# Performance work log

Hardware: AMD Instinct MI355X
Metric: run time of the kernel (lower is better)

The kernel has to match this reference:

```python
import jax, jax.numpy as jnp
import numpy as np

N_NODES = 4096
N_HEADS = 8
NEG_SLOPE = 0.2  # PyG GATConv default leaky_relu slope


def _gat_single(h, src, dst, att_src, att_dst):
    # h: [N, H, C] projected node features; src/dst: [E] (self-loops included)
    a_s = (h * att_src).sum(-1)                      # [N, H]
    a_d = (h * att_dst).sum(-1)                      # [N, H]
    e = jax.nn.leaky_relu(a_s[src] + a_d[dst], NEG_SLOPE)   # [E, H]
    m = jax.ops.segment_max(e, dst, num_segments=N_NODES)   # [N, H]
    ex = jnp.exp(e - m[dst])                         # [E, H]
    denom = jax.ops.segment_sum(ex, dst, num_segments=N_NODES)
    alpha = ex / denom[dst]                          # [E, H] (self-loops => denom > 0)
    out = jax.ops.segment_sum(alpha[:, :, None] * h[src], dst, num_segments=N_NODES)
    return out                                       # [N, H, C]


def setup_inputs() -> dict:
    key = jax.random.key(0)
    ks = jax.random.split(key, 12)
    B, T, N, F = 4, 12, N_NODES, 8
    Hg, Hl = 64, 128
    inp = {
        "x": jax.random.normal(ks[0], (B, T, N, F), jnp.float32),
        "edge_index": jax.random.randint(ks[1], (2, 65536), 0, N, jnp.int64),
        "W_gat": jax.random.normal(ks[2], (F, Hg), jnp.float32) * 0.3,
        "att_src": jax.random.normal(ks[3], (N_HEADS, Hg // N_HEADS), jnp.float32) * 0.3,
        "att_dst": jax.random.normal(ks[4], (N_HEADS, Hg // N_HEADS), jnp.float32) * 0.3,
        "b_gat": jax.random.normal(ks[5], (Hg,), jnp.float32) * 0.1,
        "W_ih": jax.random.normal(ks[6], (4 * Hl, Hg * N), jnp.float32) * 0.002,
        "W_hh": jax.random.normal(ks[7], (4 * Hl, Hl), jnp.float32) * 0.05,
        "b_ih": jax.random.normal(ks[8], (4 * Hl,), jnp.float32) * 0.05,
        "b_hh": jax.random.normal(ks[9], (4 * Hl,), jnp.float32) * 0.05,
        "W_fc": jax.random.normal(ks[10], (Hl, N * F), jnp.float32) * 0.05,
        "b_fc": jax.random.normal(ks[11], (N * F,), jnp.float32) * 0.05,
    }
    return inp


def reference(x, edge_index, W_gat, att_src, att_dst, b_gat,
              W_ih, W_hh, b_ih, b_hh, W_fc, b_fc):
    B, T, N, F = x.shape
    H = N_HEADS
    C = W_gat.shape[1] // H
    Hl = W_hh.shape[1]

    # add self-loops (PyG GATConv default add_self_loops=True)
    loop = jnp.arange(N, dtype=edge_index.dtype)
    src = jnp.concatenate([edge_index[0], loop])
    dst = jnp.concatenate([edge_index[1], loop])

    # ---- GAT over all (batch, time) graphs at once ----
    h = (x.reshape(B * T, N, F) @ W_gat).reshape(B * T, N, H, C)
    gat = jax.vmap(_gat_single, in_axes=(0, None, None, None, None))(
        h, src, dst, att_src, att_dst)                # [BT, N, H, C]
    gat = gat.reshape(B * T, N, H * C) + b_gat
    gat = jax.nn.elu(gat)                             # dropout p=0 (eval) => identity
    seq = gat.reshape(B, T, N * H * C)

    # ---- LSTM (torch gate order: i, f, g, o) ----
    def step(carry, x_t):
        hprev, cprev = carry
        gates = x_t @ W_ih.T + b_ih + hprev @ W_hh.T + b_hh   # [B, 4Hl]
        i, f, g, o = jnp.split(gates, 4, axis=-1)
        c = jax.nn.sigmoid(f) * cprev + jax.nn.sigmoid(i) * jnp.tanh(g)
        hn = jax.nn.sigmoid(o) * jnp.tanh(c)
        return (hn, c), None

    h0 = jnp.zeros((B, Hl), x.dtype)
    (h_last, _), _ = jax.lax.scan(step, (h0, h0), seq.transpose(1, 0, 2))

    out = h_last @ W_fc + b_fc
    return out.reshape(B, N, F)
```

## Files before the change

kernel.cpp:

```cpp
#include <hip/hip_runtime.h>

#define NN 4096
#define NH 8
#define BTT 48
#define KG 262144
#define NJ 512
#define HLL 128
#define ERAW 65536
#define NKC 256
#define NG  24576
#define CAP 64

typedef __attribute__((ext_vector_type(8))) short bf16x8;
typedef __attribute__((ext_vector_type(4))) float f32x4;
typedef __attribute__((ext_vector_type(8))) unsigned short ushort8;

__device__ __forceinline__ unsigned short f2bf(float f) {
  unsigned int u = __float_as_uint(f);
  u += 0x7FFFu + ((u >> 16) & 1u);
  return (unsigned short)(u >> 16);
}
__device__ __forceinline__ float bf2f(unsigned short s) {
  return __uint_as_float(((unsigned int)s) << 16);
}
__device__ __forceinline__ float4 nt_load4(const float* p) {
  f32x4 v = __builtin_nontemporal_load((const f32x4*)p);
  return float4{v[0], v[1], v[2], v[3]};
}

__global__ __launch_bounds__(256) void k_scatter(const int* __restrict__ ei, int* __restrict__ cursor,
                                                 int* __restrict__ ssrc) {
  int t = blockIdx.x * 256 + threadIdx.x;
  if (t < ERAW) {
    int s = ei[t], d = ei[ERAW + t];
    int pos = atomicAdd(&cursor[d], 1);
    ssrc[(d << 6) + pos] = s;
  } else {
    int n = t - ERAW;
    int pos = atomicAdd(&cursor[n], 1);
    ssrc[(n << 6) + pos] = n;
  }
}

__global__ __launch_bounds__(256) void k_proj(const float* __restrict__ x, const float* __restrict__ Wg,
                                              const float* __restrict__ att_s, const float* __restrict__ att_d,
                                              unsigned short* __restrict__ h, float* __restrict__ a_s,
                                              float* __restrict__ a_d) {
  __shared__ float wgs[512];
  __shared__ float ats[64], atd[64];
  int tid = threadIdx.x;
  wgs[tid] = Wg[tid];
  wgs[256 + tid] = Wg[256 + tid];
  if (tid < 64) { ats[tid] = att_s[tid]; atd[tid] = att_d[tid]; }
  __syncthreads();
  int bt = blockIdx.x >> 7;
  int inner = blockIdx.x & 127;
  int hd = tid & 7, nl = tid >> 3;
  int n = inner * 32 + nl;
  const float* xr = x + ((size_t)(bt * NN + n)) * 8;
  float4 xa = *(const float4*)xr, xb2 = *(const float4*)(xr + 4);
  float xv[8] = {xa.x, xa.y, xa.z, xa.w, xb2.x, xb2.y, xb2.z, xb2.w};
  int hb = hd * 8;
  float hv[8];
#pragma unroll
  for (int c = 0; c < 8; ++c) {
    float acc = 0.f;
#pragma unroll
    for (int f = 0; f < 8; ++f) acc += xv[f] * wgs[f * 64 + hb + c];
    hv[c] = acc;
  }
  float as = 0.f, ad = 0.f;
#pragma unroll
  for (int c = 0; c < 8; ++c) { as += hv[c] * ats[hb + c]; ad += hv[c] * atd[hb + c]; }
  int aoff = bt * (NN * NH) + n * NH + hd;
  a_s[aoff] = as;
  a_d[aoff] = ad;
  ushort8 hr;
#pragma unroll
  for (int c = 0; c < 8; ++c) hr[c] = f2bf(hv[c]);
  *(ushort8*)(h + (size_t)bt * KG + (size_t)n * 64 + hb) = hr;
}

__global__ __launch_bounds__(256) void k_gat(const unsigned short* __restrict__ h, const float* __restrict__ a_s,
                                             const float* __restrict__ a_d, const int* __restrict__ cursor,
                                             const int* __restrict__ ssrc, const float* __restrict__ b_gat,
                                             unsigned short* __restrict__ Xb) {
  int B = blockIdx.x;
  int xcd = B & 7;
  int slot = B >> 3;
  int btg = slot >> 7;
  int inner = slot & 127;
  int bt = btg * 8 + xcd;
  int tid = threadIdx.x;
  int hd = tid & 7, nl = tid >> 3;
  int n = inner * 32 + nl;
  const unsigned short* hbase = h + (size_t)bt * KG;
  const float* asb = a_s + bt * (NN * NH);
  float adn = a_d[bt * (NN * NH) + n * NH + hd];
  int deg = cursor[n];
  const int* bucket = ssrc + (n << 6);
  float ssum = 0.f;
  float o[8];
#pragma unroll
  for (int c = 0; c < 8; ++c) o[c] = 0.f;
  for (int i = 0; i < deg; ++i) {
    int s = bucket[i];
    float e = asb[s * NH + hd] + adn;
    e = (e > 0.f) ? e : 0.2f * e;
    float p = __expf(e);
    ssum += p;
    ushort8 hvv = *(const ushort8*)(hbase + (size_t)s * 64 + hd * 8);
#pragma unroll
    for (int c = 0; c < 8; ++c) o[c] += p * bf2f(hvv[c]);
  }
  float inv = 1.f / ssum;
  ushort8 r;
#pragma unroll
  for (int c = 0; c < 8; ++c) {
    float v = o[c] * inv + b_gat[hd * 8 + c];
    v = (v > 0.f) ? v : (__expf(v) - 1.f);
    r[c] = f2bf(v);
  }
  *(ushort8*)(Xb + (size_t)bt * KG + (size_t)n * 64 + hd * 8) = r;
}

__global__ __launch_bounds__(256) void k_gemm(const unsigned short* __restrict__ Xb,
                                              const float* __restrict__ Wih, float* __restrict__ Gp) {
  int tid = threadIdx.x;
  int w = tid >> 6, lane = tid & 63;
  int lm = lane & 15, kg = lane >> 4;
  int jb = blockIdx.x & 3;
  int kc = blockIdx.x >> 2;
  int j0 = jb * 128 + w * 32;
  size_t kbase = (size_t)kc * 1024 + kg * 8;

  const float* wr0 = Wih + (size_t)(j0 + lm) * KG + kbase;
  const float* wr1 = Wih + (size_t)(j0 + 16 + lm) * KG + kbase;
  const short* Xs = (const short*)Xb;
  const short* xr0 = Xs + (size_t)lm * KG + kbase;
  const short* xr1 = xr0 + (size_t)16 * KG;
  const short* xr2 = xr0 + (size_t)32 * KG;

  f32x4 acc[3][2];
#pragma unroll
  for (int mf = 0; mf < 3; ++mf)
#pragma unroll
    for (int jf = 0; jf < 2; ++jf) acc[mf][jf] = f32x4{0.f, 0.f, 0.f, 0.f};

  float4 wbuf[2][4];
  bf16x8 abuf[2][3];

  wbuf[0][0] = nt_load4(wr0);
  wbuf[0][1] = nt_load4(wr0 + 4);
  wbuf[0][2] = nt_load4(wr1);
  wbuf[0][3] = nt_load4(wr1 + 4);
  abuf[0][0] = *(const bf16x8*)(xr0);
  abuf[0][1] = *(const bf16x8*)(xr1);
  abuf[0][2] = *(const bf16x8*)(xr2);

#pragma unroll 2
  for (int t = 0; t < 32; ++t) {
    int cur = t & 1, nxt = cur ^ 1;
    if (t + 1 < 32) {
      int off = (t + 1) * 32;
      wbuf[nxt][0] = nt_load4(wr0 + off);
      wbuf[nxt][1] = nt_load4(wr0 + off + 4);
      wbuf[nxt][2] = nt_load4(wr1 + off);
      wbuf[nxt][3] = nt_load4(wr1 + off + 4);
      abuf[nxt][0] = *(const bf16x8*)(xr0 + off);
      abuf[nxt][1] = *(const bf16x8*)(xr1 + off);
      abuf[nxt][2] = *(const bf16x8*)(xr2 + off);
    }
#pragma unroll
    for (int jf = 0; jf < 2; ++jf) {
      float4 f0 = wbuf[cur][jf * 2], f1 = wbuf[cur][jf * 2 + 1];
      bf16x8 bb;
      bb[0] = (short)f2bf(f0.x); bb[1] = (short)f2bf(f0.y);
      bb[2] = (short)f2bf(f0.z); bb[3] = (short)f2bf(f0.w);
      bb[4] = (short)f2bf(f1.x); bb[5] = (short)f2bf(f1.y);
      bb[6] = (short)f2bf(f1.z); bb[7] = (short)f2bf(f1.w);
      acc[0][jf] = __builtin_amdgcn_mfma_f32_16x16x32_bf16(abuf[cur][0], bb, acc[0][jf], 0, 0, 0);
      acc[1][jf] = __builtin_amdgcn_mfma_f32_16x16x32_bf16(abuf[cur][1], bb, acc[1][jf], 0, 0, 0);
      acc[2][jf] = __builtin_amdgcn_mfma_f32_16x16x32_bf16(abuf[cur][2], bb, acc[2][jf], 0, 0, 0);
    }
  }

  float* gout = Gp + (size_t)kc * NG;
#pragma unroll
  for (int mf = 0; mf < 3; ++mf)
#pragma unroll
    for (int jf = 0; jf < 2; ++jf) {
      int j = j0 + jf * 16 + lm;
#pragma unroll
      for (int r = 0; r < 4; ++r) {
        int bt = mf * 16 + kg * 4 + r;
        gout[bt * NJ + j] = acc[mf][jf][r];
      }
    }
}

__global__ __launch_bounds__(256) void k_red1(const float* __restrict__ Gp, float* __restrict__ Gp2) {
  int idx = blockIdx.x * 256 + threadIdx.x;
  int seg = idx / NG;
  int gid = idx - seg * NG;
  const float* src = Gp + (size_t)seg * 32 * NG + gid;
  float acc = 0.f;
#pragma unroll 8
  for (int i = 0; i < 32; ++i) acc += src[(size_t)i * NG];
  Gp2[idx] = acc;
}

__global__ __launch_bounds__(512) void k_lstm(const float* __restrict__ Gp2, const float* __restrict__ Whh,
                                              const float* __restrict__ bih, const float* __restrict__ bhh,
                                              float* __restrict__ hlast) {
  __shared__ float hs[HLL];
  __shared__ float gs[NJ];
  int b = blockIdx.x, j = threadIdx.x;
  float bias = bih[j] + bhh[j];
  float w[HLL];
  const float* wr = Whh + (size_t)j * HLL;
#pragma unroll
  for (int k = 0; k < HLL; k += 4) {
    float4 v = *(const float4*)(wr + k);
    w[k] = v.x; w[k + 1] = v.y; w[k + 2] = v.z; w[k + 3] = v.w;
  }
  if (j < HLL) hs[j] = 0.f;
  float c = 0.f;
  __syncthreads();
  for (int t = 0; t < 12; ++t) {
    const float* gp = Gp2 + (size_t)(b * 12 + t) * NJ + j;
    float acc = bias;
#pragma unroll
    for (int s = 0; s < 8; ++s) acc += gp[(size_t)s * NG];
#pragma unroll
    for (int k = 0; k < HLL; ++k) acc += w[k] * hs[k];
    gs[j] = acc;
    __syncthreads();
    if (j < HLL) {
      float gi = gs[j], gf = gs[HLL + j], gg = gs[2 * HLL + j], go = gs[3 * HLL + j];
      float si = 1.f / (1.f + __expf(-gi));
      float sf = 1.f / (1.f + __expf(-gf));
      float so = 1.f / (1.f + __expf(-go));
      c = sf * c + si * tanhf(gg);
      hs[j] = so * tanhf(c);
    }
    __syncthreads();
  }
  if (j < HLL) hlast[b * HLL + j] = hs[j];
}

__global__ __launch_bounds__(256) void k_fc(const float* __restrict__ hlast, const float* __restrict__ Wfc,
                                            const float* __restrict__ bfc, float* __restrict__ out) {
  __shared__ float hl[NJ];
  int tid = threadIdx.x;
  hl[tid] = hlast[tid];
  hl[256 + tid] = hlast[256 + tid];
  __syncthreads();
  int n = blockIdx.x * 256 + tid;
  float a0 = 0.f, a1 = 0.f, a2 = 0.f, a3 = 0.f;
#pragma unroll 8
  for (int k = 0; k < HLL; ++k) {
    float wv = Wfc[(size_t)k * 32768 + n];
    a0 += hl[k] * wv;
    a1 += hl[HLL + k] * wv;
    a2 += hl[2 * HLL + k] * wv;
    a3 += hl[3 * HLL + k] * wv;
  }
  float bb = bfc[n];
  out[n] = a0 + bb;
  out[32768 + n] = a1 + bb;
  out[65536 + n] = a2 + bb;
  out[98304 + n] = a3 + bb;
}

extern "C" void kernel_launch(void* const* d_in, const int* in_sizes, int n_in,
                              void* d_out, int out_size, void* d_ws, size_t ws_size,
                              hipStream_t stream) {
  const float* x     = (const float*)d_in[0];
  const int*   ei    = (const int*)d_in[1];
  const float* Wg    = (const float*)d_in[2];
  const float* att_s = (const float*)d_in[3];
  const float* att_d = (const float*)d_in[4];
  const float* b_gat = (const float*)d_in[5];
  const float* Wih   = (const float*)d_in[6];
  const float* Whh   = (const float*)d_in[7];
  const float* bih   = (const float*)d_in[8];
  const float* bhh   = (const float*)d_in[9];
  const float* Wfc   = (const float*)d_in[10];
  const float* bfc   = (const float*)d_in[11];
  float* out = (float*)d_out;

  char* ws = (char*)d_ws;
  unsigned short* h  = (unsigned short*)(ws);
  float* a_s         = (float*)(ws + 25165824);
  float* a_d         = (float*)(ws + 31457280);
  unsigned short* Xb = (unsigned short*)(ws + 37748736);
  float* Gp          = (float*)(ws + 62914560);
  int* ssrc          = (int*)(ws + 87031808);
  float* Gp2         = (float*)(ws + 88080384);
  float* hlast       = (float*)(ws + 88866816);
  int* cursor        = (int*)(ws + 88868864);

  hipMemsetAsync(cursor, 0, NN * sizeof(int), stream);
  hipLaunchKernelGGL(k_scatter, dim3(272),      dim3(256), 0, stream, ei, cursor, ssrc);
  hipLaunchKernelGGL(k_proj,    dim3(48 * 128), dim3(256), 0, stream, x, Wg, att_s, att_d, h, a_s, a_d);
  hipLaunchKernelGGL(k_gat,     dim3(48 * 128), dim3(256), 0, stream, h, a_s, a_d, cursor, ssrc, b_gat, Xb);
  hipLaunchKernelGGL(k_gemm,    dim3(1024),     dim3(256), 0, stream, Xb, Wih, Gp);
  hipLaunchKernelGGL(k_red1,    dim3(768),      dim3(256), 0, stream, Gp, Gp2);
  hipLaunchKernelGGL(k_lstm,    dim3(4),        dim3(512), 0, stream, Gp2, Whh, bih, bhh, hlast);
  hipLaunchKernelGGL(k_fc,      dim3(128),      dim3(256), 0, stream, hlast, Wfc, bfc, out);
}
```

Measured before the change: 312.5 us.

## Fuse scatter into projection kernel and reduce GEMM split-K with atomics

The edge scatter and accumulator zeroing are merged into the projection kernel as extra blocks, removing one launch. The split-K GEMM now atomically adds partial results directly into a single gate buffer instead of writing 256 partial slabs that a separate reduction kernel and the LSTM then summed. This drops the k_red1 launch and the large partial-sum traffic, at the cost of many float atomics contending on the same addresses and a nondeterministic summation order.

```diff
diff --git a/kernel.cpp b/kernel.cpp
--- a/kernel.cpp
+++ b/kernel.cpp
@@ -9,7 +9,6 @@
 #define ERAW 65536
 #define NKC 256
 #define NG  24576
-#define CAP 64
 
 typedef __attribute__((ext_vector_type(8))) short bf16x8;
 typedef __attribute__((ext_vector_type(4))) float f32x4;
@@ -28,33 +27,36 @@
   return float4{v[0], v[1], v[2], v[3]};
 }
 
-__global__ __launch_bounds__(256) void k_scatter(const int* __restrict__ ei, int* __restrict__ cursor,
-                                                 int* __restrict__ ssrc) {
-  int t = blockIdx.x * 256 + threadIdx.x;
-  if (t < ERAW) {
-    int s = ei[t], d = ei[ERAW + t];
-    int pos = atomicAdd(&cursor[d], 1);
-    ssrc[(d << 6) + pos] = s;
-  } else {
-    int n = t - ERAW;
-    int pos = atomicAdd(&cursor[n], 1);
-    ssrc[(n << 6) + pos] = n;
-  }
-}
-
-__global__ __launch_bounds__(256) void k_proj(const float* __restrict__ x, const float* __restrict__ Wg,
-                                              const float* __restrict__ att_s, const float* __restrict__ att_d,
-                                              unsigned short* __restrict__ h, float* __restrict__ a_s,
-                                              float* __restrict__ a_d) {
+__global__ __launch_bounds__(256) void k_sp(const float* __restrict__ x, const float* __restrict__ Wg,
+                                            const float* __restrict__ att_s, const float* __restrict__ att_d,
+                                            const int* __restrict__ ei, int* __restrict__ cursor,
+                                            int* __restrict__ ssrc, float* __restrict__ G,
+                                            unsigned short* __restrict__ h, float* __restrict__ a_s,
+                                            float* __restrict__ a_d) {
+  int tid = threadIdx.x;
+  int bid = blockIdx.x;
+  if (bid >= 6144) {
+    int t = (bid - 6144) * 256 + tid;
+    if (t < NG) G[t] = 0.f;
+    if (t < ERAW) {
+      int s = ei[t], d = ei[ERAW + t];
+      int pos = atomicAdd(&cursor[d], 1);
+      ssrc[(d << 6) + pos] = s;
+    } else {
+      int n = t - ERAW;
+      int pos = atomicAdd(&cursor[n], 1);
+      ssrc[(n << 6) + pos] = n;
+    }
+    return;
+  }
   __shared__ float wgs[512];
   __shared__ float ats[64], atd[64];
-  int tid = threadIdx.x;
   wgs[tid] = Wg[tid];
   wgs[256 + tid] = Wg[256 + tid];
   if (tid < 64) { ats[tid] = att_s[tid]; atd[tid] = att_d[tid]; }
   __syncthreads();
-  int bt = blockIdx.x >> 7;
-  int inner = blockIdx.x & 127;
+  int bt = bid >> 7;
+  int inner = bid & 127;
   int hd = tid & 7, nl = tid >> 3;
   int n = inner * 32 + nl;
   const float* xr = x + ((size_t)(bt * NN + n)) * 8;
@@ -125,7 +127,7 @@
 }
 
 __global__ __launch_bounds__(256) void k_gemm(const unsigned short* __restrict__ Xb,
-                                              const float* __restrict__ Wih, float* __restrict__ Gp) {
+                                              const float* __restrict__ Wih, float* __restrict__ G) {
   int tid = threadIdx.x;
   int w = tid >> 6, lane = tid & 63;
   int lm = lane & 15, kg = lane >> 4;
@@ -185,7 +187,6 @@
     }
   }
 
-  float* gout = Gp + (size_t)kc * NG;
 #pragma unroll
   for (int mf = 0; mf < 3; ++mf)
 #pragma unroll
@@ -194,23 +195,12 @@
 #pragma unroll
       for (int r = 0; r < 4; ++r) {
         int bt = mf * 16 + kg * 4 + r;
-        gout[bt * NJ + j] = acc[mf][jf][r];
+        atomicAdd(&G[bt * NJ + j], acc[mf][jf][r]);
       }
     }
 }
 
-__global__ __launch_bounds__(256) void k_red1(const float* __restrict__ Gp, float* __restrict__ Gp2) {
-  int idx = blockIdx.x * 256 + threadIdx.x;
-  int seg = idx / NG;
-  int gid = idx - seg * NG;
-  const float* src = Gp + (size_t)seg * 32 * NG + gid;
-  float acc = 0.f;
-#pragma unroll 8
-  for (int i = 0; i < 32; ++i) acc += src[(size_t)i * NG];
-  Gp2[idx] = acc;
-}
-
-__global__ __launch_bounds__(512) void k_lstm(const float* __restrict__ Gp2, const float* __restrict__ Whh,
+__global__ __launch_bounds__(512) void k_lstm(const float* __restrict__ G, const float* __restrict__ Whh,
                                               const float* __restrict__ bih, const float* __restrict__ bhh,
                                               float* __restrict__ hlast) {
   __shared__ float hs[HLL];
@@ -228,10 +218,7 @@
   float c = 0.f;
   __syncthreads();
   for (int t = 0; t < 12; ++t) {
-    const float* gp = Gp2 + (size_t)(b * 12 + t) * NJ + j;
-    float acc = bias;
-#pragma unroll
-    for (int s = 0; s < 8; ++s) acc += gp[(size_t)s * NG];
+    float acc = G[(size_t)(b * 12 + t) * NJ + j] + bias;
 #pragma unroll
     for (int k = 0; k < HLL; ++k) acc += w[k] * hs[k];
     gs[j] = acc;
@@ -295,18 +282,15 @@
   float* a_s         = (float*)(ws + 25165824);
   float* a_d         = (float*)(ws + 31457280);
   unsigned short* Xb = (unsigned short*)(ws + 37748736);
-  float* Gp          = (float*)(ws + 62914560);
-  int* ssrc          = (int*)(ws + 87031808);
-  float* Gp2         = (float*)(ws + 88080384);
-  float* hlast       = (float*)(ws + 88866816);
-  int* cursor        = (int*)(ws + 88868864);
+  int* ssrc          = (int*)(ws + 62914560);
+  float* G           = (float*)(ws + 63963136);
+  float* hlast       = (float*)(ws + 64061440);
+  int* cursor        = (int*)(ws + 64063488);
 
   hipMemsetAsync(cursor, 0, NN * sizeof(int), stream);
-  hipLaunchKernelGGL(k_scatter, dim3(272),      dim3(256), 0, stream, ei, cursor, ssrc);
-  hipLaunchKernelGGL(k_proj,    dim3(48 * 128), dim3(256), 0, stream, x, Wg, att_s, att_d, h, a_s, a_d);
-  hipLaunchKernelGGL(k_gat,     dim3(48 * 128), dim3(256), 0, stream, h, a_s, a_d, cursor, ssrc, b_gat, Xb);
-  hipLaunchKernelGGL(k_gemm,    dim3(1024),     dim3(256), 0, stream, Xb, Wih, Gp);
-  hipLaunchKernelGGL(k_red1,    dim3(768),      dim3(256), 0, stream, Gp, Gp2);
-  hipLaunchKernelGGL(k_lstm,    dim3(4),        dim3(512), 0, stream, Gp2, Whh, bih, bhh, hlast);
-  hipLaunchKernelGGL(k_fc,      dim3(128),      dim3(256), 0, stream, hlast, Wfc, bfc, out);
-}
+  hipLaunchKernelGGL(k_sp,   dim3(6416),     dim3(256), 0, stream, x, Wg, att_s, att_d, ei, cursor, ssrc, G, h, a_s, a_d);
+  hipLaunchKernelGGL(k_gat,  dim3(48 * 128), dim3(256), 0, stream, h, a_s, a_d, cursor, ssrc, b_gat, Xb);
+  hipLaunchKernelGGL(k_gemm, dim3(1024),     dim3(256), 0, stream, Xb, Wih, G);
+  hipLaunchKernelGGL(k_lstm, dim3(4),        dim3(512), 0, stream, G, Whh, bih, bhh, hlast);
+  hipLaunchKernelGGL(k_fc,   dim3(128),      dim3(256), 0, stream, hlast, Wfc, bfc, out);
+}
```

Result: faster. 286.0 us, median of 3 (-8.5%).
